# Performance work log

Hardware: AMD Instinct MI355X
Metric: run time of the kernel (lower is better)

The kernel has to match this reference:

```python
import jax, jax.numpy as jnp
import numpy as np

N_NODES = 50000


def sage_conv(x, src, dst, Wl, bl, Wr, n_nodes):
    # PyG SAGEConv (aggr='mean', root_weight=True, bias on lin_l):
    #   out = lin_l(mean_{j in N(i)} x_j) + lin_r(x_i)
    msg = x[src]  # [E, d] gather
    s = jax.ops.segment_sum(msg, dst, num_segments=n_nodes)  # [N, d]
    cnt = jax.ops.segment_sum(jnp.ones((src.shape[0], 1), x.dtype), dst,
                              num_segments=n_nodes)  # [N, 1]
    agg = s / jnp.maximum(cnt, 1.0)
    return agg @ Wl.T + bl + x @ Wr.T


def setup_inputs() -> dict:
    key = jax.random.key(0)
    ks = jax.random.split(key, 8)
    in_c, hid_c, out_c = 256, 256, 2
    x = jax.random.normal(ks[0], (N_NODES, in_c), dtype=jnp.float32)
    edge_index = jax.random.randint(ks[1], (2, 800000), 0, N_NODES, dtype=jnp.int64)
    def lin(k, fan_out, fan_in):
        bound = 1.0 / np.sqrt(fan_in)
        return jax.random.uniform(k, (fan_out, fan_in), jnp.float32, -bound, bound)
    return {
        "x": x,
        "edge_index": edge_index,
        "W1l": lin(ks[2], hid_c, in_c),
        "b1": jnp.zeros((hid_c,), jnp.float32),
        "W1r": lin(ks[3], hid_c, in_c),
        "W2l": lin(ks[4], out_c, hid_c),
        "b2": jnp.zeros((out_c,), jnp.float32),
        "W2r": lin(ks[5], out_c, hid_c),
    }


def reference(x, edge_index, W1l, b1, W1r, W2l, b2, W2r):
    src, dst = edge_index[0], edge_index[1]
    h = sage_conv(x, src, dst, W1l, b1, W1r, N_NODES)
    h = jax.nn.relu(h)
    # dropout is identity in eval mode (training=False)
    out = sage_conv(h, src, dst, W2l, b2, W2r, N_NODES)
    return jax.nn.log_softmax(out, axis=1)
```

## Files before the change

kernel.cpp:

```cpp
#include <hip/hip_runtime.h>
#include <math.h>

#define DIM 256
#define GBM 128
#define GBN 128
#define GBK 64
#define LDS_K 72
#define SCHUNK 1024

typedef short bf16x8 __attribute__((ext_vector_type(8)));
typedef float f32x4 __attribute__((ext_vector_type(4)));

__device__ __forceinline__ ushort f2bf(float f) {
  uint u = __float_as_uint(f);
  u += 0x7fffu + ((u >> 16) & 1u);
  return (ushort)(u >> 16);
}
__device__ __forceinline__ float bf2f(uint bits) {
  return __uint_as_float(bits << 16);
}

__global__ __launch_bounds__(256) void prep_kernel(
    const float4* __restrict__ x4, ushort* __restrict__ xb, int n4,
    const float* __restrict__ Wl, const float* __restrict__ Wr,
    const float* __restrict__ W2l, const float* __restrict__ W2r,
    ushort* __restrict__ Wb, ushort* __restrict__ W2b,
    const int* __restrict__ dst, int* __restrict__ deg, int E) {
  const int t0 = blockIdx.x * blockDim.x + threadIdx.x;
  const int stride = gridDim.x * blockDim.x;
  for (int i = t0; i < n4; i += stride) {
    const float4 v = x4[i];
    ushort4 o;
    o.x = f2bf(v.x); o.y = f2bf(v.y); o.z = f2bf(v.z); o.w = f2bf(v.w);
    *(ushort4*)&xb[i * 4] = o;
  }
  if (t0 < 131072) {
    const int n = t0 >> 9, k = t0 & 511;
    const float v = (k < 256) ? Wl[n * 256 + k] : Wr[n * 256 + (k - 256)];
    Wb[t0] = f2bf(v);
  } else if (t0 < 135168) {
    const int w2 = t0 - 131072;
    const int row = w2 >> 8, k = w2 & 255;
    float v = 0.f;
    if (row < 2)      v = W2l[row * 256 + k];
    else if (row < 4) v = W2r[(row - 2) * 256 + k];
    W2b[w2] = f2bf(v);
  }
  for (int e = t0; e < E; e += stride) atomicAdd(&deg[dst[e]], 1);
}

__global__ __launch_bounds__(256) void scan_partial(
    const int* __restrict__ deg, int* __restrict__ bsum, int M) {
  const int base = blockIdx.x * SCHUNK + threadIdx.x * 4;
  int s = 0;
  if (base + 3 < M) {
    const int4 v = *(const int4*)(deg + base);
    s = v.x + v.y + v.z + v.w;
  } else {
    for (int j = 0; j < 4; ++j) if (base + j < M) s += deg[base + j];
  }
  #pragma unroll
  for (int off = 32; off; off >>= 1) s += __shfl_xor(s, off);
  __shared__ int ws[4];
  if ((threadIdx.x & 63) == 0) ws[threadIdx.x >> 6] = s;
  __syncthreads();
  if (threadIdx.x == 0) bsum[blockIdx.x] = ws[0] + ws[1] + ws[2] + ws[3];
}

__global__ __launch_bounds__(1024) void scan_sums(
    int* __restrict__ bsum, int nb) {
  __shared__ int sh[1024];
  const int t = threadIdx.x;
  const int orig = (t < nb) ? bsum[t] : 0;
  sh[t] = orig;
  __syncthreads();
  for (int off = 1; off < 1024; off <<= 1) {
    const int v = sh[t];
    const int u = (t >= off) ? sh[t - off] : 0;
    __syncthreads();
    sh[t] = v + u;
    __syncthreads();
  }
  if (t < nb) bsum[t] = sh[t] - orig;
}

__global__ __launch_bounds__(256) void scan_finalize(
    const int* __restrict__ deg, const int* __restrict__ bsum,
    int* __restrict__ rowptr, int* __restrict__ fill,
    float* __restrict__ invc, int M) {
  const int t = threadIdx.x;
  const int lane = t & 63;
  const int wid = t >> 6;
  const int base = blockIdx.x * SCHUNK + t * 4;
  int d[4];
  #pragma unroll
  for (int j = 0; j < 4; ++j) d[j] = (base + j < M) ? deg[base + j] : 0;
  const int tsum = d[0] + d[1] + d[2] + d[3];
  int v = tsum;
  #pragma unroll
  for (int off = 1; off < 64; off <<= 1) {
    const int u = __shfl_up(v, off);
    if (lane >= off) v += u;
  }
  __shared__ int wtot[4];
  if (lane == 63) wtot[wid] = v;
  __syncthreads();
  int wbase = 0;
  for (int w = 0; w < wid; ++w) wbase += wtot[w];
  int run = bsum[blockIdx.x] + wbase + v - tsum;
  #pragma unroll
  for (int j = 0; j < 4; ++j) {
    const int idx = base + j;
    if (idx < M) {
      rowptr[idx] = run;
      fill[idx]   = run;
      invc[idx]   = 1.0f / fmaxf((float)d[j], 1.0f);
      run += d[j];
      if (idx == M - 1) rowptr[M] = run;
    }
  }
}

__global__ __launch_bounds__(256) void scatter_edges(
    const int* __restrict__ src, const int* __restrict__ dst,
    int* __restrict__ fill, int* __restrict__ esrc, int E) {
  int e = blockIdx.x * blockDim.x + threadIdx.x;
  if (e < E) {
    const int pos = atomicAdd(&fill[dst[e]], 1);
    esrc[pos] = src[e];
  }
}

__global__ __launch_bounds__(256) void gather1(
    const ushort* __restrict__ xb, const int* __restrict__ esrc,
    const int* __restrict__ rowptr, const float* __restrict__ invc,
    ushort* __restrict__ aggb, int M) {
  const int lane = threadIdx.x & 63;
  const int wave = threadIdx.x >> 6;
  const int half = lane >> 5;
  const int fl   = lane & 31;
  const int i = blockIdx.x * 4 + wave;
  if (i >= M) return;
  const int k0 = rowptr[i];
  const int k1 = rowptr[i + 1];
  float s0 = 0.f, s1 = 0.f, s2 = 0.f, s3 = 0.f;
  float s4 = 0.f, s5 = 0.f, s6 = 0.f, s7 = 0.f;

#define ACC(v)                                                  \
  do {                                                          \
    s0 += bf2f((v).x & 0xffffu); s1 += bf2f((v).x >> 16);       \
    s2 += bf2f((v).y & 0xffffu); s3 += bf2f((v).y >> 16);       \
    s4 += bf2f((v).z & 0xffffu); s5 += bf2f((v).z >> 16);       \
    s6 += bf2f((v).w & 0xffffu); s7 += bf2f((v).w >> 16);       \
  } while (0)

  int k = k0;
  for (; k + 7 < k1; k += 8) {
    const int e0 = esrc[k + 0 + half];
    const int e1 = esrc[k + 2 + half];
    const int e2 = esrc[k + 4 + half];
    const int e3 = esrc[k + 6 + half];
    const uint4 v0 = *(const uint4*)(xb + (size_t)e0 * DIM + fl * 8);
    const uint4 v1 = *(const uint4*)(xb + (size_t)e1 * DIM + fl * 8);
    const uint4 v2 = *(const uint4*)(xb + (size_t)e2 * DIM + fl * 8);
    const uint4 v3 = *(const uint4*)(xb + (size_t)e3 * DIM + fl * 8);
    ACC(v0); ACC(v1); ACC(v2); ACC(v3);
  }
  for (; k + 1 < k1; k += 2) {
    const int e = esrc[k + half];
    const uint4 v = *(const uint4*)(xb + (size_t)e * DIM + fl * 8);
    ACC(v);
  }
  if (k < k1 && half == 0) {
    const uint4 v = *(const uint4*)(xb + (size_t)esrc[k] * DIM + fl * 8);
    ACC(v);
  }
#undef ACC

  s0 += __shfl_xor(s0, 32); s1 += __shfl_xor(s1, 32);
  s2 += __shfl_xor(s2, 32); s3 += __shfl_xor(s3, 32);
  s4 += __shfl_xor(s4, 32); s5 += __shfl_xor(s5, 32);
  s6 += __shfl_xor(s6, 32); s7 += __shfl_xor(s7, 32);

  if (half == 0) {
    const float inv = invc[i];
    uint4 o;
    o.x = (uint)f2bf(s0 * inv) | ((uint)f2bf(s1 * inv) << 16);
    o.y = (uint)f2bf(s2 * inv) | ((uint)f2bf(s3 * inv) << 16);
    o.z = (uint)f2bf(s4 * inv) | ((uint)f2bf(s5 * inv) << 16);
    o.w = (uint)f2bf(s6 * inv) | ((uint)f2bf(s7 * inv) << 16);
    *(uint4*)(aggb + (size_t)i * DIM + fl * 8) = o;
  }
}

__global__ __launch_bounds__(256) void gemm1_mfma(
    const ushort* __restrict__ Ab, const ushort* __restrict__ Xb,
    const ushort* __restrict__ Wb, const float* __restrict__ b1,
    ushort* __restrict__ Hb, int M) {
  __shared__ __align__(16) ushort As[GBM * LDS_K];
  __shared__ __align__(16) ushort Bs[GBN * LDS_K];

  const int tid  = threadIdx.x;
  const int lane = tid & 63;
  const int wave = tid >> 6;
  const int wm = wave >> 1, wn = wave & 1;
  const int row0 = blockIdx.x * GBM;
  const int col0 = blockIdx.y * GBN;

  const int lr = tid >> 3;
  const int lc = tid & 7;

  const int frow = lane & 15;
  const int fk   = (lane >> 4) * 8;

  f32x4 acc[4][4] = {};
  uint4 ga[4], gb[4];

#define LOADR(T)                                                               \
  do {                                                                         \
    const ushort* srcA = ((T) < 4) ? Ab : Xb;                                  \
    const int kofs = ((T) * GBK) & 255;                                        \
    _Pragma("unroll")                                                          \
    for (int i_ = 0; i_ < 4; ++i_) {                                           \
      const int r_ = lr + i_ * 32;                                             \
      const int grow_ = row0 + r_;                                             \
      ga[i_] = (grow_ < M)                                                     \
          ? *(const uint4*)(srcA + (size_t)grow_ * DIM + kofs + lc * 8)        \
          : make_uint4(0, 0, 0, 0);                                            \
      gb[i_] = *(const uint4*)(Wb + (size_t)(col0 + r_) * 512 + (T) * GBK + lc * 8); \
    }                                                                          \
  } while (0)

  LOADR(0);
  #pragma unroll
  for (int t = 0; t < 8; ++t) {
    #pragma unroll
    for (int i = 0; i < 4; ++i) {
      const int r = lr + i * 32;
      *(uint4*)&As[r * LDS_K + lc * 8] = ga[i];
      *(uint4*)&Bs[r * LDS_K + lc * 8] = gb[i];
    }
    __syncthreads();
    if (t < 7) {
      switch (t + 1) {
        case 1: LOADR(1); break;
        case 2: LOADR(2); break;
        case 3: LOADR(3); break;
        case 4: LOADR(4); break;
        case 5: LOADR(5); break;
        case 6: LOADR(6); break;
        case 7: LOADR(7); break;
      }
    }
    #pragma unroll
    for (int s = 0; s < 2; ++s) {
      bf16x8 a[4], b[4];
      #pragma unroll
      for (int i = 0; i < 4; ++i)
        a[i] = *(const bf16x8*)&As[(wm * 64 + i * 16 + frow) * LDS_K + s * 32 + fk];
      #pragma unroll
      for (int j = 0; j < 4; ++j)
        b[j] = *(const bf16x8*)&Bs[(wn * 64 + j * 16 + frow) * LDS_K + s * 32 + fk];
      #pragma unroll
      for (int i = 0; i < 4; ++i)
        #pragma unroll
        for (int j = 0; j < 4; ++j)
          acc[i][j] = __builtin_amdgcn_mfma_f32_16x16x32_bf16(a[i], b[j], acc[i][j], 0, 0, 0);
    }
    __syncthreads();
  }
#undef LOADR

  #pragma unroll
  for (int i = 0; i < 4; ++i) {
    #pragma unroll
    for (int j = 0; j < 4; ++j) {
      const int col = col0 + wn * 64 + j * 16 + (lane & 15);
      const float bias = b1[col];
      #pragma unroll
      for (int r = 0; r < 4; ++r) {
        const int grow = row0 + wm * 64 + i * 16 + (lane >> 4) * 4 + r;
        if (grow < M) {
          const float v = fmaxf(acc[i][j][r] + bias, 0.f);
          Hb[(size_t)grow * DIM + col] = f2bf(v);
        }
      }
    }
  }
}

__global__ __launch_bounds__(256) void proj2_mfma(
    const ushort* __restrict__ Hb, const ushort* __restrict__ W2b,
    float* __restrict__ Y4v, int M) {
  const int lane = threadIdx.x & 63;
  const int wave = threadIdx.x >> 6;
  const int row0 = (blockIdx.x * 4 + wave) * 16;
  if (row0 >= M) return;
  const int frow = lane & 15;
  const int fk   = (lane >> 4) * 8;

  f32x4 acc = {};
  #pragma unroll
  for (int s = 0; s < 8; ++s) {
    bf16x8 a = {};
    if (row0 + frow < M)
      a = *(const bf16x8*)(Hb + (size_t)(row0 + frow) * DIM + s * 32 + fk);
    const bf16x8 b = *(const bf16x8*)(W2b + frow * DIM + s * 32 + fk);
    acc = __builtin_amdgcn_mfma_f32_16x16x32_bf16(a, b, acc, 0, 0, 0);
  }
  const int col = lane & 15;
  if (col < 4) {
    #pragma unroll
    for (int r = 0; r < 4; ++r) {
      const int row = row0 + (lane >> 4) * 4 + r;
      if (row < M) Y4v[(size_t)row * 4 + col] = acc[r];
    }
  }
}

__global__ __launch_bounds__(256) void layer2_finalize(
    const float2* __restrict__ Y2, const int* __restrict__ esrc,
    const int* __restrict__ rowptr, const float* __restrict__ invc,
    const float* __restrict__ b2, float* __restrict__ out, int M) {
  int i = blockIdx.x * blockDim.x + threadIdx.x;
  if (i < M) {
    const int k0 = rowptr[i];
    const int k1 = rowptr[i + 1];
    float a0 = 0.f, a1 = 0.f;
    int k = k0;
    for (; k + 3 < k1; k += 4) {
      const int e0 = esrc[k], e1 = esrc[k + 1], e2 = esrc[k + 2], e3 = esrc[k + 3];
      const float2 y0 = Y2[2 * (size_t)e0];
      const float2 y1 = Y2[2 * (size_t)e1];
      const float2 y2 = Y2[2 * (size_t)e2];
      const float2 y3 = Y2[2 * (size_t)e3];
      a0 += y0.x + y1.x + y2.x + y3.x;
      a1 += y0.y + y1.y + y2.y + y3.y;
    }
    for (; k < k1; ++k) {
      const float2 y = Y2[2 * (size_t)esrc[k]];
      a0 += y.x; a1 += y.y;
    }
    const float inv = invc[i];
    const float2 yr = Y2[2 * (size_t)i + 1];
    const float o0 = a0 * inv + yr.x + b2[0];
    const float o1 = a1 * inv + yr.y + b2[1];
    const float m = fmaxf(o0, o1);
    const float lse = m + logf(expf(o0 - m) + expf(o1 - m));
    out[2 * i + 0] = o0 - lse;
    out[2 * i + 1] = o1 - lse;
  }
}

extern "C" void kernel_launch(void* const* d_in, const int* in_sizes, int n_in,
                              void* d_out, int out_size, void* d_ws, size_t ws_size,
                              hipStream_t stream) {
  const float* x   = (const float*)d_in[0];
  const int*   ei  = (const int*)d_in[1];
  const float* W1l = (const float*)d_in[2];
  const float* b1  = (const float*)d_in[3];
  const float* W1r = (const float*)d_in[4];
  const float* W2l = (const float*)d_in[5];
  const float* b2  = (const float*)d_in[6];
  const float* W2r = (const float*)d_in[7];

  const int E = in_sizes[1] / 2;
  const int M = in_sizes[0] / DIM;
  const int* src = ei;
  const int* dst = ei + E;

  char* ws = (char*)d_ws;
  size_t off = 0;
  ushort* xb   = (ushort*)(ws + off); off += (size_t)M * DIM * 2;
  ushort* aggb = (ushort*)(ws + off); off += (size_t)M * DIM * 2;
  ushort* Hb   = (ushort*)(ws + off); off += (size_t)M * DIM * 2;
  ushort* Wb   = (ushort*)(ws + off); off += (size_t)256 * 512 * 2;
  ushort* W2b  = (ushort*)(ws + off); off += (size_t)16 * 256 * 2;
  float* Y4v   = (float*)(ws + off);  off += (size_t)M * 4 * 4;
  float* invc  = (float*)(ws + off);  off += (size_t)M * 4;
  int* deg     = (int*)(ws + off);    off += (size_t)M * 4;
  int* fill    = (int*)(ws + off);    off += (size_t)M * 4;
  int* rowptr  = (int*)(ws + off);    off += (size_t)(M + 1) * 4;
  int* bsum    = (int*)(ws + off);    off += 1024 * 4;
  int* esrc    = (int*)(ws + off);    off += (size_t)E * 4;

  hipMemsetAsync(deg, 0, (size_t)M * 4, stream);

  const int EB = (E + 255) / 256;
  const int NB = (M + SCHUNK - 1) / SCHUNK;

  prep_kernel<<<2048, 256, 0, stream>>>((const float4*)x, xb, M * DIM / 4,
                                        W1l, W1r, W2l, W2r, Wb, W2b, dst, deg, E);
  scan_partial<<<NB, 256, 0, stream>>>(deg, bsum, M);
  scan_sums<<<1, 1024, 0, stream>>>(bsum, NB);
  scan_finalize<<<NB, 256, 0, stream>>>(deg, bsum, rowptr, fill, invc, M);
  scatter_edges<<<EB, 256, 0, stream>>>(src, dst, fill, esrc, E);
  gather1<<<(M + 3) / 4, 256, 0, stream>>>(xb, esrc, rowptr, invc, aggb, M);

  dim3 g1((M + GBM - 1) / GBM, DIM / GBN);
  gemm1_mfma<<<g1, 256, 0, stream>>>(aggb, xb, Wb, b1, Hb, M);

  proj2_mfma<<<(M / 16 + 3) / 4 + 1, 256, 0, stream>>>(Hb, W2b, Y4v, M);
  layer2_finalize<<<(M + 255) / 256, 256, 0, stream>>>(
      (const float2*)Y4v, esrc, rowptr, invc, b2, (float*)d_out, M);
}
```

Before: 318.8 us.

## Use direct global-to-LDS loads in gemm1 and stage epilogue through swizzled LDS

The first-layer GEMM now loads A and W tiles straight into shared memory with global_load_lds, replacing the register-staged prefetch and its padded layout. The output tile is written into a swizzled LDS buffer and then stored to global memory as coalesced 16-byte rows, instead of scattered 2-byte stores. In exchange, the load of the next tile no longer overlaps with compute. The unpadded 64-element LDS rows may cause bank conflicts on fragment reads. The row bounds check on A loads is gone, so the last block can read past M.

```diff
diff --git a/kernel.cpp b/kernel.cpp
--- a/kernel.cpp
+++ b/kernel.cpp
@@ -5,7 +5,6 @@
 #define GBM 128
 #define GBN 128
 #define GBK 64
-#define LDS_K 72
 #define SCHUNK 1024
 
 typedef short bf16x8 __attribute__((ext_vector_type(8)));
@@ -18,6 +17,12 @@
 }
 __device__ __forceinline__ float bf2f(uint bits) {
   return __uint_as_float(bits << 16);
+}
+
+__device__ __forceinline__ void async_copy16(const ushort* g, ushort* l) {
+  __builtin_amdgcn_global_load_lds(
+      (const __attribute__((address_space(1))) unsigned int*)g,
+      (__attribute__((address_space(3))) unsigned int*)l, 16, 0, 0);
 }
 
 __global__ __launch_bounds__(256) void prep_kernel(
@@ -197,8 +202,9 @@
     const ushort* __restrict__ Ab, const ushort* __restrict__ Xb,
     const ushort* __restrict__ Wb, const float* __restrict__ b1,
     ushort* __restrict__ Hb, int M) {
-  __shared__ __align__(16) ushort As[GBM * LDS_K];
-  __shared__ __align__(16) ushort Bs[GBN * LDS_K];
+  __shared__ __align__(16) ushort lds[2 * GBM * GBK];
+  ushort* As = lds;
+  ushort* Bs = lds + GBM * GBK;
 
   const int tid  = threadIdx.x;
   const int lane = tid & 63;
@@ -207,60 +213,38 @@
   const int row0 = blockIdx.x * GBM;
   const int col0 = blockIdx.y * GBN;
 
-  const int lr = tid >> 3;
-  const int lc = tid & 7;
+  const int lsub = lane >> 3;
+  const int lk   = lane & 7;
 
   const int frow = lane & 15;
   const int fk   = (lane >> 4) * 8;
 
   f32x4 acc[4][4] = {};
-  uint4 ga[4], gb[4];
-
-#define LOADR(T)                                                               \
-  do {                                                                         \
-    const ushort* srcA = ((T) < 4) ? Ab : Xb;                                  \
-    const int kofs = ((T) * GBK) & 255;                                        \
-    _Pragma("unroll")                                                          \
-    for (int i_ = 0; i_ < 4; ++i_) {                                           \
-      const int r_ = lr + i_ * 32;                                             \
-      const int grow_ = row0 + r_;                                             \
-      ga[i_] = (grow_ < M)                                                     \
-          ? *(const uint4*)(srcA + (size_t)grow_ * DIM + kofs + lc * 8)        \
-          : make_uint4(0, 0, 0, 0);                                            \
-      gb[i_] = *(const uint4*)(Wb + (size_t)(col0 + r_) * 512 + (T) * GBK + lc * 8); \
-    }                                                                          \
-  } while (0)
-
-  LOADR(0);
-  #pragma unroll
+
   for (int t = 0; t < 8; ++t) {
+    const int kt = t * GBK;
+    const ushort* srcA = (t < 4) ? Ab : Xb;
+    const int kofs = kt & 255;
     #pragma unroll
     for (int i = 0; i < 4; ++i) {
-      const int r = lr + i * 32;
-      *(uint4*)&As[r * LDS_K + lc * 8] = ga[i];
-      *(uint4*)&Bs[r * LDS_K + lc * 8] = gb[i];
+      const int rbase = i * 32 + wave * 8;
+      const int r = rbase + lsub;
+      async_copy16(srcA + (size_t)(row0 + r) * DIM + kofs + lk * 8,
+                   &As[rbase * GBK]);
+      async_copy16(Wb + (size_t)(col0 + r) * 512 + kt + lk * 8,
+                   &Bs[rbase * GBK]);
     }
     __syncthreads();
-    if (t < 7) {
-      switch (t + 1) {
-        case 1: LOADR(1); break;
-        case 2: LOADR(2); break;
-        case 3: LOADR(3); break;
-        case 4: LOADR(4); break;
-        case 5: LOADR(5); break;
-        case 6: LOADR(6); break;
-        case 7: LOADR(7); break;
-      }
-    }
+
     #pragma unroll
     for (int s = 0; s < 2; ++s) {
       bf16x8 a[4], b[4];
       #pragma unroll
       for (int i = 0; i < 4; ++i)
-        a[i] = *(const bf16x8*)&As[(wm * 64 + i * 16 + frow) * LDS_K + s * 32 + fk];
+        a[i] = *(const bf16x8*)&As[(wm * 64 + i * 16 + frow) * GBK + s * 32 + fk];
       #pragma unroll
       for (int j = 0; j < 4; ++j)
-        b[j] = *(const bf16x8*)&Bs[(wn * 64 + j * 16 + frow) * LDS_K + s * 32 + fk];
+        b[j] = *(const bf16x8*)&Bs[(wn * 64 + j * 16 + frow) * GBK + s * 32 + fk];
       #pragma unroll
       for (int i = 0; i < 4; ++i)
         #pragma unroll
@@ -269,22 +253,28 @@
     }
     __syncthreads();
   }
-#undef LOADR
 
   #pragma unroll
   for (int i = 0; i < 4; ++i) {
     #pragma unroll
     for (int j = 0; j < 4; ++j) {
-      const int col = col0 + wn * 64 + j * 16 + (lane & 15);
-      const float bias = b1[col];
+      const int col = wn * 64 + j * 16 + frow;
+      const float bias = b1[col0 + col];
       #pragma unroll
       for (int r = 0; r < 4; ++r) {
-        const int grow = row0 + wm * 64 + i * 16 + (lane >> 4) * 4 + r;
-        if (grow < M) {
-          const float v = fmaxf(acc[i][j][r] + bias, 0.f);
-          Hb[(size_t)grow * DIM + col] = f2bf(v);
-        }
+        const int row = wm * 64 + i * 16 + (lane >> 4) * 4 + r;
+        lds[row * 128 + (col ^ ((row & 7) << 3))] =
+            f2bf(fmaxf(acc[i][j][r] + bias, 0.f));
       }
+    }
+  }
+  __syncthreads();
+  for (int c = tid; c < 128 * 16; c += 256) {
+    const int row = c >> 4;
+    const int grow = row0 + row;
+    if (grow < M) {
+      const uint4 v = *(const uint4*)&lds[row * 128 + (((c & 15) ^ (row & 7)) * 8)];
+      *(uint4*)(Hb + (size_t)grow * DIM + col0 + (c & 15) * 8) = v;
     }
   }
 }
```

Result: faster. 284.6 us (-10.7%).
